# Optimization experiments

Measured on AMD Instinct MI355X. Metric: run time of the kernel, lower is better.

The kernel has to match this reference:

```python
import jax, jax.numpy as jnp
import numpy as np

BN_EPS = 1e-3  # Keras BatchNormalization default epsilon

def setup_inputs() -> dict:
    key = jax.random.key(0)
    ks = jax.random.split(key, 6)
    B, H, W, C = 8, 128, 128, 128
    s = 0.05  # small init scale for weights
    return {
        "x1": jax.random.normal(ks[0], (B, H, W, C), jnp.float32),
        "x2": jax.random.normal(ks[1], (B, H, W, C), jnp.float32),
        "Wq": jax.random.normal(ks[2], (C, C), jnp.float32) * s,
        "Wk": jax.random.normal(ks[3], (C, C), jnp.float32) * s,
        "Wv": jax.random.normal(ks[4], (C, C), jnp.float32) * s,
        "Ws": jax.random.normal(ks[5], (C, C), jnp.float32) * s,
        "bs": jnp.zeros((C,), jnp.float32),
        "scale": jnp.ones((1,), jnp.float32),   # layers.Attention use_scale=True, init 1
        "gamma": jnp.ones((C,), jnp.float32),
        "beta": jnp.zeros((C,), jnp.float32),
        "mu": jnp.zeros((C,), jnp.float32),
        "var": jnp.ones((C,), jnp.float32),
    }


def reference(x1, x2, Wq, Wk, Wv, Ws, bs, scale, gamma, beta, mu, var):
    # x1, x2: [B,H,W,C].  1x1 convs with relu == per-pixel channel matmul.
    q = jax.nn.relu(jnp.einsum('bhwc,cd->bhwd', x1, Wq))  # [B,H,W,C]
    k = jax.nn.relu(jnp.einsum('bhwc,cd->bhwd', x1, Wk))
    v = jax.nn.relu(jnp.einsum('bhwc,cd->bhwd', x2, Wv))
    # After transpose [0,3,1,2], Keras Attention batches over (B,C):
    # seq axis = H (rows), feature dim = W (cols). Fold the transposes into einsum.
    scores = scale[0] * jnp.einsum('bhwc,bgwc->bchg', q, k)  # [B,C,H,H]
    attn = jax.nn.softmax(scores, axis=-1)
    # attn @ v over row axis g, then implicit transpose back to NHWC.
    o = jnp.einsum('bchg,bgwc->bhwc', attn, v)  # [B,H,W,C]
    # sigmoid 1x1 conv (with bias), then inference-mode BatchNorm.
    g = jax.nn.sigmoid(jnp.einsum('bhwc,cd->bhwd', o, Ws) + bs)
    g = gamma * (g - mu) * jax.lax.rsqrt(var + BN_EPS) + beta
    # gated residual
    return x1 + x2 * g
```

## Files before the change

### kernel.cpp

```cpp
#include <hip/hip_runtime.h>

typedef unsigned int u32;
typedef unsigned short u16;
typedef u16 u16x4 __attribute__((ext_vector_type(4)));
typedef u16 u16x8 __attribute__((ext_vector_type(8)));
typedef u32 u32x2 __attribute__((ext_vector_type(2)));
typedef u32 u32x4 __attribute__((ext_vector_type(4)));
typedef __bf16 bf16x8 __attribute__((ext_vector_type(8)));
typedef float f32x4 __attribute__((ext_vector_type(4)));

#define LDK 136
#define TIDX(r, c) ((r) * LDK + ((c) ^ (((r) & 3) << 5)))
#define MFMA(a, b, c) __builtin_amdgcn_mfma_f32_16x16x32_bf16(a, b, c, 0, 0, 0)

__device__ __forceinline__ u16 f2b(float f) {
  u32 u = __builtin_bit_cast(u32, f);
  u = (u + 0x7fffu + ((u >> 16) & 1u)) >> 16;
  return (u16)u;
}
__device__ __forceinline__ float b2f(u16 h) {
  u32 u = ((u32)h) << 16;
  return __builtin_bit_cast(float, u);
}
__device__ __forceinline__ u32 pk2(float lo, float hi) {
  return (u32)f2b(lo) | ((u32)f2b(hi) << 16);
}

__global__ void wprep(const float* __restrict__ Wq, const float* __restrict__ Wk,
                      const float* __restrict__ Wv, const float* __restrict__ Ws,
                      u16* __restrict__ wT) {
  const float* srcs[4] = {Wq, Wk, Wv, Ws};
  const float* s = srcs[blockIdx.x];
  u16* d = wT + (size_t)blockIdx.x * 16384;
  for (int idx = threadIdx.x; idx < 16384; idx += 256) {
    int i = idx >> 7, j = idx & 127;
    d[j * 128 + i] = f2b(s[idx]);
  }
}

__global__ __launch_bounds__(256, 4)
void qkv_kernel(const float* __restrict__ x1, const float* __restrict__ x2,
                const u16* __restrict__ wT,
                u16* __restrict__ q_t, u16* __restrict__ k_t, u16* __restrict__ v_t) {
  __shared__ u16 Xs[128 * LDK];

  const int t = threadIdx.x;
  const int bid = blockIdx.x;
  const int xs = bid & 7;
  const int m = (bid >> 3) % 3;
  const int bh = (bid / 24) * 8 + xs;
  const int b = bh >> 7, h = bh & 127;
  const size_t pixbase = (size_t)bh * 16384;
  const size_t obase = (size_t)b * 2097152 + (size_t)h * 128;

  const float* xin = (m == 2) ? x2 : x1;
  u16* dst = (m == 0) ? q_t : (m == 1) ? k_t : v_t;

  const int lane = t & 63, wave = t >> 6;
  const int lrow = lane & 15, lq = lane >> 4;
  const int nstrip = wave * 32;

#pragma unroll
  for (int j = 0; j < 8; ++j) {
    int lin = j * 256 + t;
    int w = lin >> 4, c0 = (lin & 15) << 3;
    f32x4 a0 = *(const f32x4*)&xin[pixbase + lin * 8];
    f32x4 a1 = *(const f32x4*)&xin[pixbase + lin * 8 + 4];
    u16x8 p;
#pragma unroll
    for (int i = 0; i < 4; ++i) { p[i] = f2b(a0[i]); p[4 + i] = f2b(a1[i]); }
    *(u16x8*)&Xs[TIDX(w, c0)] = p;
  }

  const u16* wb = wT + (size_t)m * 16384;
  bf16x8 w0[4], w1[4];
#pragma unroll
  for (int kk = 0; kk < 4; ++kk) {
    int ko = kk * 32 + lq * 8;
    w0[kk] = *(const bf16x8*)&wb[(nstrip + lrow) * 128 + ko];
    w1[kk] = *(const bf16x8*)&wb[(nstrip + 16 + lrow) * 128 + ko];
  }
  __syncthreads();

  f32x4 acc[8][2];
#pragma unroll
  for (int mt = 0; mt < 8; ++mt) {
    acc[mt][0] = (f32x4){0.f, 0.f, 0.f, 0.f};
    acc[mt][1] = (f32x4){0.f, 0.f, 0.f, 0.f};
  }
#pragma unroll
  for (int kk = 0; kk < 4; ++kk) {
    int ko = kk * 32 + lq * 8;
#pragma unroll
    for (int mt = 0; mt < 8; ++mt) {
      bf16x8 a = *(const bf16x8*)&Xs[TIDX(mt * 16 + lrow, ko)];
      acc[mt][0] = MFMA(a, w0[kk], acc[mt][0]);
      acc[mt][1] = MFMA(a, w1[kk], acc[mt][1]);
    }
  }
  __syncthreads();

#pragma unroll
  for (int mt = 0; mt < 8; ++mt) {
    int w0i = mt * 16 + lq * 4;
#pragma unroll
    for (int nt = 0; nt < 2; ++nt) {
      int c = nstrip + nt * 16 + lrow;
      u32x2 p;
      p[0] = pk2(fmaxf(acc[mt][nt][0], 0.f), fmaxf(acc[mt][nt][1], 0.f));
      p[1] = pk2(fmaxf(acc[mt][nt][2], 0.f), fmaxf(acc[mt][nt][3], 0.f));
      *(u32x2*)&Xs[TIDX(c, w0i)] = p;
    }
  }
  __syncthreads();

#pragma unroll
  for (int j = 0; j < 8; ++j) {
    int c = j * 16 + (t >> 4), wv = (t & 15) * 8;
    *(u16x8*)&dst[obase + (size_t)c * 16384 + wv] = *(const u16x8*)&Xs[TIDX(c, wv)];
  }
}

__global__ __launch_bounds__(256, 3)
void attn_kernel(u16* __restrict__ q_t, const u16* __restrict__ k_t,
                 const u16* __restrict__ v_t, const float* __restrict__ scale_p) {
  __shared__ u16 Ks[128 * LDK];

  const int t = threadIdx.x;
  const size_t base = (size_t)blockIdx.x * 16384;

  const int lane = t & 63, wave = t >> 6;
  const int lrow = lane & 15, lq = lane >> 4;
  const int hstrip = wave * 32;
  const float scl = scale_p[0];

  bf16x8 q0[4], q1[4];
#pragma unroll
  for (int kk = 0; kk < 4; ++kk) {
    int ko = kk * 32 + lq * 8;
    q0[kk] = *(const bf16x8*)&q_t[base + (hstrip + lrow) * 128 + ko];
    q1[kk] = *(const bf16x8*)&q_t[base + (hstrip + 16 + lrow) * 128 + ko];
  }
#pragma unroll
  for (int j = 0; j < 8; ++j) {
    int lin = j * 256 + t;
    int r = lin >> 4, c0 = (lin & 15) << 3;
    *(u16x8*)&Ks[TIDX(r, c0)] = *(const u16x8*)&k_t[base + lin * 8];
  }
  __syncthreads();

  f32x4 acc[8][2];
#pragma unroll
  for (int mt = 0; mt < 8; ++mt) {
    acc[mt][0] = (f32x4){0.f, 0.f, 0.f, 0.f};
    acc[mt][1] = (f32x4){0.f, 0.f, 0.f, 0.f};
  }
#pragma unroll
  for (int kk = 0; kk < 4; ++kk) {
    int ko = kk * 32 + lq * 8;
#pragma unroll
    for (int mt = 0; mt < 8; ++mt) {
      bf16x8 a = *(const bf16x8*)&Ks[TIDX(mt * 16 + lrow, ko)];
      acc[mt][0] = MFMA(a, q0[kk], acc[mt][0]);
      acc[mt][1] = MFMA(a, q1[kk], acc[mt][1]);
    }
  }

  const int w0v = (t & 15) * 8, g0 = (t >> 4) * 8;
  u16x8 vv[8];
#pragma unroll
  for (int i = 0; i < 8; ++i)
    vv[i] = *(const u16x8*)&v_t[base + (size_t)(g0 + i) * 128 + w0v];

  float inv[2];
#pragma unroll
  for (int nt = 0; nt < 2; ++nt) {
    float mx = -1e30f;
#pragma unroll
    for (int mt = 0; mt < 8; ++mt)
#pragma unroll
      for (int r = 0; r < 4; ++r) {
        acc[mt][nt][r] *= scl;
        mx = fmaxf(mx, acc[mt][nt][r]);
      }
    mx = fmaxf(mx, __shfl_xor(mx, 16));
    mx = fmaxf(mx, __shfl_xor(mx, 32));
    float s = 0.f;
#pragma unroll
    for (int mt = 0; mt < 8; ++mt)
#pragma unroll
      for (int r = 0; r < 4; ++r) {
        float e = __expf(acc[mt][nt][r] - mx);
        acc[mt][nt][r] = e;
        s += e;
      }
    s += __shfl_xor(s, 16);
    s += __shfl_xor(s, 32);
    inv[nt] = 1.f / s;
  }

  u32 pk[8][2][2];
#pragma unroll
  for (int mt = 0; mt < 8; ++mt)
#pragma unroll
    for (int nt = 0; nt < 2; ++nt) {
      pk[mt][nt][0] = pk2(acc[mt][nt][0] * inv[nt], acc[mt][nt][1] * inv[nt]);
      pk[mt][nt][1] = pk2(acc[mt][nt][2] * inv[nt], acc[mt][nt][3] * inv[nt]);
    }
  __syncthreads();

#pragma unroll
  for (int j = 0; j < 8; ++j) {
    u16x8 tv;
#pragma unroll
    for (int i = 0; i < 8; ++i) tv[i] = vv[i][j];
    *(u16x8*)&Ks[TIDX(w0v + j, g0)] = tv;
  }
  __syncthreads();

  const int s01 = lrow + 32 * (lq & 1);
  const int s23 = s01 + 16;
  const bool hi = (lq & 2);
#pragma unroll
  for (int kk = 0; kk < 4; ++kk) {
    int ko = kk * 32 + lq * 8;
    u32x4 bd[2];
#pragma unroll
    for (int nt = 0; nt < 2; ++nt) {
      u32 a0 = pk[2 * kk][nt][0], a1 = pk[2 * kk][nt][1];
      u32 c0 = pk[2 * kk + 1][nt][0], c1 = pk[2 * kk + 1][nt][1];
      u32 l0 = (u32)__shfl((int)a0, s01), h0 = (u32)__shfl((int)c0, s01);
      u32 l1 = (u32)__shfl((int)a1, s01), h1 = (u32)__shfl((int)c1, s01);
      u32 l2 = (u32)__shfl((int)a0, s23), h2 = (u32)__shfl((int)c0, s23);
      u32 l3 = (u32)__shfl((int)a1, s23), h3 = (u32)__shfl((int)c1, s23);
      bd[nt][0] = hi ? h0 : l0;
      bd[nt][1] = hi ? h1 : l1;
      bd[nt][2] = hi ? h2 : l2;
      bd[nt][3] = hi ? h3 : l3;
    }
    bf16x8 bb0 = __builtin_bit_cast(bf16x8, bd[0]);
    bf16x8 bb1 = __builtin_bit_cast(bf16x8, bd[1]);
    if (kk == 0) {
#pragma unroll
      for (int mt = 0; mt < 8; ++mt) {
        acc[mt][0] = (f32x4){0.f, 0.f, 0.f, 0.f};
        acc[mt][1] = (f32x4){0.f, 0.f, 0.f, 0.f};
      }
    }
#pragma unroll
    for (int mt = 0; mt < 8; ++mt) {
      bf16x8 a = *(const bf16x8*)&Ks[TIDX(mt * 16 + lrow, ko)];
      acc[mt][0] = MFMA(a, bb0, acc[mt][0]);
      acc[mt][1] = MFMA(a, bb1, acc[mt][1]);
    }
  }
  __syncthreads();

#pragma unroll
  for (int mt = 0; mt < 8; ++mt) {
    int w0i = mt * 16 + lq * 4;
#pragma unroll
    for (int nt = 0; nt < 2; ++nt) {
      int hh = hstrip + nt * 16 + lrow;
      u32x2 p;
      p[0] = pk2(acc[mt][nt][0], acc[mt][nt][1]);
      p[1] = pk2(acc[mt][nt][2], acc[mt][nt][3]);
      *(u32x2*)&Ks[TIDX(hh, w0i)] = p;
    }
  }
  __syncthreads();
#pragma unroll
  for (int j = 0; j < 8; ++j) {
    int hh = j * 16 + (t >> 4), wv = (t & 15) * 8;
    *(u16x8*)&q_t[base + hh * 128 + wv] = *(const u16x8*)&Ks[TIDX(hh, wv)];
  }
}

__global__ __launch_bounds__(256, 4)
void final_kernel(const u16* __restrict__ o_t, const u16* __restrict__ wsT,
                  const float* __restrict__ x1, const float* __restrict__ x2,
                  const float* __restrict__ bs, const float* __restrict__ gamma,
                  const float* __restrict__ beta, const float* __restrict__ mu,
                  const float* __restrict__ var, float* __restrict__ out) {
  __shared__ u16 Os[128 * LDK];
  __shared__ float bnA[128], bnB[128], bsf[128];

  const int t = threadIdx.x;
  const int bh = blockIdx.x;
  const int b = bh >> 7, h = bh & 127;
  const size_t obase = (size_t)b * 2097152 + (size_t)h * 128;
  const size_t pixbase = (size_t)bh * 16384;

  if (t < 128) {
    float a = gamma[t] * rsqrtf(var[t] + 1e-3f);
    bnA[t] = a;
    bnB[t] = beta[t] - mu[t] * a;
    bsf[t] = bs[t];
  }
  {
    int cb = (t >> 4) * 8, w0 = (t & 15) * 8;
    u16 ov[8][8];
#pragma unroll
    for (int i = 0; i < 8; ++i)
      *(u16x8*)&ov[i][0] = *(const u16x8*)&o_t[obase + (size_t)(cb + i) * 16384 + w0];
#pragma unroll
    for (int j = 0; j < 8; ++j) {
      u16x8 tv;
#pragma unroll
      for (int i = 0; i < 8; ++i) tv[i] = ov[i][j];
      *(u16x8*)&Os[TIDX(w0 + j, cb)] = tv;
    }
  }
  __syncthreads();

  const int lane = t & 63, wave = t >> 6;
  const int lrow = lane & 15, lq = lane >> 4;
  const int wstrip = wave * 32;

  f32x4 acc[8][2];
#pragma unroll
  for (int mt = 0; mt < 8; ++mt) {
    acc[mt][0] = (f32x4){0.f, 0.f, 0.f, 0.f};
    acc[mt][1] = (f32x4){0.f, 0.f, 0.f, 0.f};
  }
#pragma unroll
  for (int kk = 0; kk < 4; ++kk) {
    int ko = kk * 32 + lq * 8;
    bf16x8 b0 = *(const bf16x8*)&Os[TIDX(wstrip + lrow, ko)];
    bf16x8 b1 = *(const bf16x8*)&Os[TIDX(wstrip + 16 + lrow, ko)];
#pragma unroll
    for (int mt = 0; mt < 8; ++mt) {
      bf16x8 a = *(const bf16x8*)&wsT[(mt * 16 + lrow) * 128 + ko];
      acc[mt][0] = MFMA(a, b0, acc[mt][0]);
      acc[mt][1] = MFMA(a, b1, acc[mt][1]);
    }
  }

#pragma unroll
  for (int mt = 0; mt < 8; ++mt) {
    int d0 = mt * 16 + lq * 4;
    f32x4 A4 = *(const f32x4*)&bnA[d0];
    f32x4 B4 = *(const f32x4*)&bnB[d0];
    f32x4 S4 = *(const f32x4*)&bsf[d0];
#pragma unroll
    for (int nt = 0; nt < 2; ++nt) {
      int w = wstrip + nt * 16 + lrow;
      size_t off = pixbase + (size_t)w * 128 + d0;
      f32x4 a1v = *(const f32x4*)&x1[off];
      f32x4 a2v = *(const f32x4*)&x2[off];
      f32x4 r;
#pragma unroll
      for (int r4 = 0; r4 < 4; ++r4) {
        float sv = acc[mt][nt][r4] + S4[r4];
        float sg = 1.f / (1.f + __expf(-sv));
        float g = A4[r4] * sg + B4[r4];
        r[r4] = a1v[r4] + a2v[r4] * g;
      }
      *(f32x4*)&out[off] = r;
    }
  }
}

extern "C" void kernel_launch(void* const* d_in, const int* in_sizes, int n_in,
                              void* d_out, int out_size, void* d_ws, size_t ws_size,
                              hipStream_t stream) {
  const float* x1 = (const float*)d_in[0];
  const float* x2 = (const float*)d_in[1];
  const float* Wq = (const float*)d_in[2];
  const float* Wk = (const float*)d_in[3];
  const float* Wv = (const float*)d_in[4];
  const float* Ws = (const float*)d_in[5];
  const float* bs = (const float*)d_in[6];
  const float* scale = (const float*)d_in[7];
  const float* gamma = (const float*)d_in[8];
  const float* beta = (const float*)d_in[9];
  const float* mu = (const float*)d_in[10];
  const float* var = (const float*)d_in[11];
  float* outp = (float*)d_out;

  u16* q_t = (u16*)d_ws;
  u16* k_t = q_t + 16777216;
  u16* v_t = k_t + 16777216;
  u16* wT = v_t + 16777216;

  wprep<<<dim3(4), dim3(256), 0, stream>>>(Wq, Wk, Wv, Ws, wT);
  qkv_kernel<<<dim3(3072), dim3(256), 0, stream>>>(x1, x2, wT, q_t, k_t, v_t);
  attn_kernel<<<dim3(1024), dim3(256), 0, stream>>>(q_t, k_t, v_t, scale);
  final_kernel<<<dim3(1024), dim3(256), 0, stream>>>(q_t, wT + 3 * 16384, x1, x2, bs,
                                                     gamma, beta, mu, var, outp);
}
```

Before: 322.8 us.

## Split qkv and final kernel blocks into half-row tiles for higher occupancy

Both the QKV projection and the final gating kernel now process 64 pixels of a row per block instead of 128. This halves LDS use and accumulator registers, doubles the grid, and raises launch bounds to 8 blocks per CU. The aim is more latency hiding on the memory-bound fp32 loads and stores. In exchange, the final kernel's weight loads are split across waves by output-channel strip, the qkv epilogue uses an unswizzled LDS layout with narrower writes, and global stores for o_t/q_t rows become 64-element halves.

```diff
diff --git a/kernel.cpp b/kernel.cpp
--- a/kernel.cpp
+++ b/kernel.cpp
@@ -38,20 +38,21 @@
   }
 }
 
-__global__ __launch_bounds__(256, 4)
+__global__ __launch_bounds__(256, 8)
 void qkv_kernel(const float* __restrict__ x1, const float* __restrict__ x2,
                 const u16* __restrict__ wT,
                 u16* __restrict__ q_t, u16* __restrict__ k_t, u16* __restrict__ v_t) {
-  __shared__ u16 Xs[128 * LDK];
+  __shared__ u16 Xs[64 * LDK];
 
   const int t = threadIdx.x;
   const int bid = blockIdx.x;
   const int xs = bid & 7;
-  const int m = (bid >> 3) % 3;
-  const int bh = (bid / 24) * 8 + xs;
+  const int mh = (bid >> 3) % 6;
+  const int m = mh % 3, half = mh / 3;
+  const int bh = (bid / 48) * 8 + xs;
   const int b = bh >> 7, h = bh & 127;
-  const size_t pixbase = (size_t)bh * 16384;
-  const size_t obase = (size_t)b * 2097152 + (size_t)h * 128;
+  const size_t pixbase = (size_t)bh * 16384 + half * 8192;
+  const size_t obase = (size_t)b * 2097152 + (size_t)h * 128 + half * 64;
 
   const float* xin = (m == 2) ? x2 : x1;
   u16* dst = (m == 0) ? q_t : (m == 1) ? k_t : v_t;
@@ -61,7 +62,7 @@
   const int nstrip = wave * 32;
 
 #pragma unroll
-  for (int j = 0; j < 8; ++j) {
+  for (int j = 0; j < 4; ++j) {
     int lin = j * 256 + t;
     int w = lin >> 4, c0 = (lin & 15) << 3;
     f32x4 a0 = *(const f32x4*)&xin[pixbase + lin * 8];
@@ -82,9 +83,9 @@
   }
   __syncthreads();
 
-  f32x4 acc[8][2];
-#pragma unroll
-  for (int mt = 0; mt < 8; ++mt) {
+  f32x4 acc[4][2];
+#pragma unroll
+  for (int mt = 0; mt < 4; ++mt) {
     acc[mt][0] = (f32x4){0.f, 0.f, 0.f, 0.f};
     acc[mt][1] = (f32x4){0.f, 0.f, 0.f, 0.f};
   }
@@ -92,7 +93,7 @@
   for (int kk = 0; kk < 4; ++kk) {
     int ko = kk * 32 + lq * 8;
 #pragma unroll
-    for (int mt = 0; mt < 8; ++mt) {
+    for (int mt = 0; mt < 4; ++mt) {
       bf16x8 a = *(const bf16x8*)&Xs[TIDX(mt * 16 + lrow, ko)];
       acc[mt][0] = MFMA(a, w0[kk], acc[mt][0]);
       acc[mt][1] = MFMA(a, w1[kk], acc[mt][1]);
@@ -101,7 +102,7 @@
   __syncthreads();
 
 #pragma unroll
-  for (int mt = 0; mt < 8; ++mt) {
+  for (int mt = 0; mt < 4; ++mt) {
     int w0i = mt * 16 + lq * 4;
 #pragma unroll
     for (int nt = 0; nt < 2; ++nt) {
@@ -109,15 +110,18 @@
       u32x2 p;
       p[0] = pk2(fmaxf(acc[mt][nt][0], 0.f), fmaxf(acc[mt][nt][1], 0.f));
       p[1] = pk2(fmaxf(acc[mt][nt][2], 0.f), fmaxf(acc[mt][nt][3], 0.f));
-      *(u32x2*)&Xs[TIDX(c, w0i)] = p;
-    }
-  }
-  __syncthreads();
-
-#pragma unroll
-  for (int j = 0; j < 8; ++j) {
-    int c = j * 16 + (t >> 4), wv = (t & 15) * 8;
-    *(u16x8*)&dst[obase + (size_t)c * 16384 + wv] = *(const u16x8*)&Xs[TIDX(c, wv)];
+      *(u32x2*)&Xs[c * 68 + w0i] = p;
+    }
+  }
+  __syncthreads();
+
+#pragma unroll
+  for (int j = 0; j < 4; ++j) {
+    int c = j * 32 + (t >> 3), wv = (t & 7) * 8;
+    u32x2 lo = *(const u32x2*)&Xs[c * 68 + wv];
+    u32x2 hi = *(const u32x2*)&Xs[c * 68 + wv + 4];
+    u32x4 full = {lo[0], lo[1], hi[0], hi[1]};
+    *(u32x4*)&dst[obase + (size_t)c * 16384 + wv] = full;
   }
 }
 
@@ -276,20 +280,21 @@
   }
 }
 
-__global__ __launch_bounds__(256, 4)
+__global__ __launch_bounds__(256, 8)
 void final_kernel(const u16* __restrict__ o_t, const u16* __restrict__ wsT,
                   const float* __restrict__ x1, const float* __restrict__ x2,
                   const float* __restrict__ bs, const float* __restrict__ gamma,
                   const float* __restrict__ beta, const float* __restrict__ mu,
                   const float* __restrict__ var, float* __restrict__ out) {
-  __shared__ u16 Os[128 * LDK];
+  __shared__ u16 Os[64 * LDK];
   __shared__ float bnA[128], bnB[128], bsf[128];
 
   const int t = threadIdx.x;
-  const int bh = blockIdx.x;
+  const int bid = blockIdx.x;
+  const int bh = bid >> 1, half = bid & 1;
   const int b = bh >> 7, h = bh & 127;
-  const size_t obase = (size_t)b * 2097152 + (size_t)h * 128;
-  const size_t pixbase = (size_t)bh * 16384;
+  const size_t obase = (size_t)b * 2097152 + (size_t)h * 128 + half * 64;
+  const size_t pixbase = (size_t)bh * 16384 + half * 8192;
 
   if (t < 128) {
     float a = gamma[t] * rsqrtf(var[t] + 1e-3f);
@@ -298,28 +303,29 @@
     bsf[t] = bs[t];
   }
   {
-    int cb = (t >> 4) * 8, w0 = (t & 15) * 8;
-    u16 ov[8][8];
+    int c0 = (t >> 4) * 8, w0 = (t & 15) * 4;
+    u16x4 ov[8];
 #pragma unroll
     for (int i = 0; i < 8; ++i)
-      *(u16x8*)&ov[i][0] = *(const u16x8*)&o_t[obase + (size_t)(cb + i) * 16384 + w0];
-#pragma unroll
-    for (int j = 0; j < 8; ++j) {
+      ov[i] = *(const u16x4*)&o_t[obase + (size_t)(c0 + i) * 16384 + w0];
+#pragma unroll
+    for (int j = 0; j < 4; ++j) {
       u16x8 tv;
 #pragma unroll
       for (int i = 0; i < 8; ++i) tv[i] = ov[i][j];
-      *(u16x8*)&Os[TIDX(w0 + j, cb)] = tv;
+      *(u16x8*)&Os[TIDX(w0 + j, c0)] = tv;
     }
   }
   __syncthreads();
 
   const int lane = t & 63, wave = t >> 6;
   const int lrow = lane & 15, lq = lane >> 4;
-  const int wstrip = wave * 32;
-
-  f32x4 acc[8][2];
-#pragma unroll
-  for (int mt = 0; mt < 8; ++mt) {
+  const int dstrip = (wave >> 1) * 64;
+  const int wstrip = (wave & 1) * 32;
+
+  f32x4 acc[4][2];
+#pragma unroll
+  for (int mt = 0; mt < 4; ++mt) {
     acc[mt][0] = (f32x4){0.f, 0.f, 0.f, 0.f};
     acc[mt][1] = (f32x4){0.f, 0.f, 0.f, 0.f};
   }
@@ -329,16 +335,16 @@
     bf16x8 b0 = *(const bf16x8*)&Os[TIDX(wstrip + lrow, ko)];
     bf16x8 b1 = *(const bf16x8*)&Os[TIDX(wstrip + 16 + lrow, ko)];
 #pragma unroll
-    for (int mt = 0; mt < 8; ++mt) {
-      bf16x8 a = *(const bf16x8*)&wsT[(mt * 16 + lrow) * 128 + ko];
+    for (int mt = 0; mt < 4; ++mt) {
+      bf16x8 a = *(const bf16x8*)&wsT[(dstrip + mt * 16 + lrow) * 128 + ko];
       acc[mt][0] = MFMA(a, b0, acc[mt][0]);
       acc[mt][1] = MFMA(a, b1, acc[mt][1]);
     }
   }
 
 #pragma unroll
-  for (int mt = 0; mt < 8; ++mt) {
-    int d0 = mt * 16 + lq * 4;
+  for (int mt = 0; mt < 4; ++mt) {
+    int d0 = dstrip + mt * 16 + lq * 4;
     f32x4 A4 = *(const f32x4*)&bnA[d0];
     f32x4 B4 = *(const f32x4*)&bnB[d0];
     f32x4 S4 = *(const f32x4*)&bsf[d0];
@@ -384,8 +390,8 @@
   u16* wT = v_t + 16777216;
 
   wprep<<<dim3(4), dim3(256), 0, stream>>>(Wq, Wk, Wv, Ws, wT);
-  qkv_kernel<<<dim3(3072), dim3(256), 0, stream>>>(x1, x2, wT, q_t, k_t, v_t);
+  qkv_kernel<<<dim3(6144), dim3(256), 0, stream>>>(x1, x2, wT, q_t, k_t, v_t);
   attn_kernel<<<dim3(1024), dim3(256), 0, stream>>>(q_t, k_t, v_t, scale);
-  final_kernel<<<dim3(1024), dim3(256), 0, stream>>>(q_t, wT + 3 * 16384, x1, x2, bs,
+  final_kernel<<<dim3(2048), dim3(256), 0, stream>>>(q_t, wT + 3 * 16384, x1, x2, bs,
                                                      gamma, beta, mu, var, outp);
 }
```

After: 344.3 us. 6.7% more time.

## Load projection input fragments directly from global memory, skipping LDS staging

Applied to the files above, without the earlier changes.

The QKV projection kernel no longer stages the input tile in shared memory. Each wave now reads its own 32 pixel rows straight from global memory into MFMA A-fragments and converts them to bf16 in registers. It streams weight B-fragments from global for all 128 output channels, and the work split changes from channel strips to pixel strips. This drops one LDS round-trip and two barriers. In exchange, the global loads are strided per lane and less coalesced, and weights are re-read from global (likely L1/L2 hits) with no latency hiding.

```diff
diff --git a/kernel.cpp b/kernel.cpp
--- a/kernel.cpp
+++ b/kernel.cpp
@@ -58,57 +58,49 @@
 
   const int lane = t & 63, wave = t >> 6;
   const int lrow = lane & 15, lq = lane >> 4;
-  const int nstrip = wave * 32;
-
-#pragma unroll
-  for (int j = 0; j < 8; ++j) {
-    int lin = j * 256 + t;
-    int w = lin >> 4, c0 = (lin & 15) << 3;
-    f32x4 a0 = *(const f32x4*)&xin[pixbase + lin * 8];
-    f32x4 a1 = *(const f32x4*)&xin[pixbase + lin * 8 + 4];
-    u16x8 p;
-#pragma unroll
-    for (int i = 0; i < 4; ++i) { p[i] = f2b(a0[i]); p[4 + i] = f2b(a1[i]); }
-    *(u16x8*)&Xs[TIDX(w, c0)] = p;
-  }
-
   const u16* wb = wT + (size_t)m * 16384;
-  bf16x8 w0[4], w1[4];
-#pragma unroll
-  for (int kk = 0; kk < 4; ++kk) {
-    int ko = kk * 32 + lq * 8;
-    w0[kk] = *(const bf16x8*)&wb[(nstrip + lrow) * 128 + ko];
-    w1[kk] = *(const bf16x8*)&wb[(nstrip + 16 + lrow) * 128 + ko];
-  }
-  __syncthreads();
-
-  f32x4 acc[8][2];
-#pragma unroll
-  for (int mt = 0; mt < 8; ++mt) {
-    acc[mt][0] = (f32x4){0.f, 0.f, 0.f, 0.f};
-    acc[mt][1] = (f32x4){0.f, 0.f, 0.f, 0.f};
-  }
-#pragma unroll
-  for (int kk = 0; kk < 4; ++kk) {
-    int ko = kk * 32 + lq * 8;
-#pragma unroll
-    for (int mt = 0; mt < 8; ++mt) {
-      bf16x8 a = *(const bf16x8*)&Xs[TIDX(mt * 16 + lrow, ko)];
-      acc[mt][0] = MFMA(a, w0[kk], acc[mt][0]);
-      acc[mt][1] = MFMA(a, w1[kk], acc[mt][1]);
-    }
-  }
-  __syncthreads();
-
-#pragma unroll
-  for (int mt = 0; mt < 8; ++mt) {
-    int w0i = mt * 16 + lq * 4;
-#pragma unroll
-    for (int nt = 0; nt < 2; ++nt) {
-      int c = nstrip + nt * 16 + lrow;
+
+  const float* arow0 = &xin[pixbase + (size_t)(wave * 32 + lrow) * 128];
+  const float* arow1 = arow0 + 16 * 128;
+
+  f32x4 acc[2][8];
+#pragma unroll
+  for (int mt = 0; mt < 2; ++mt)
+#pragma unroll
+    for (int ns = 0; ns < 8; ++ns) acc[mt][ns] = (f32x4){0.f, 0.f, 0.f, 0.f};
+
+#pragma unroll
+  for (int kk = 0; kk < 4; ++kk) {
+    int ko = kk * 32 + lq * 8;
+    f32x4 u00 = *(const f32x4*)&arow0[ko];
+    f32x4 u01 = *(const f32x4*)&arow0[ko + 4];
+    f32x4 u10 = *(const f32x4*)&arow1[ko];
+    f32x4 u11 = *(const f32x4*)&arow1[ko + 4];
+    u16x8 pa0, pa1;
+#pragma unroll
+    for (int i = 0; i < 4; ++i) {
+      pa0[i] = f2b(u00[i]); pa0[4 + i] = f2b(u01[i]);
+      pa1[i] = f2b(u10[i]); pa1[4 + i] = f2b(u11[i]);
+    }
+    bf16x8 a0 = __builtin_bit_cast(bf16x8, pa0);
+    bf16x8 a1 = __builtin_bit_cast(bf16x8, pa1);
+#pragma unroll
+    for (int ns = 0; ns < 8; ++ns) {
+      bf16x8 bfrag = *(const bf16x8*)&wb[(ns * 16 + lrow) * 128 + ko];
+      acc[0][ns] = MFMA(a0, bfrag, acc[0][ns]);
+      acc[1][ns] = MFMA(a1, bfrag, acc[1][ns]);
+    }
+  }
+
+#pragma unroll
+  for (int mt = 0; mt < 2; ++mt) {
+    int w0i = wave * 32 + mt * 16 + lq * 4;
+#pragma unroll
+    for (int ns = 0; ns < 8; ++ns) {
+      int c = ns * 16 + lrow;
       u32x2 p;
-      p[0] = pk2(fmaxf(acc[mt][nt][0], 0.f), fmaxf(acc[mt][nt][1], 0.f));
-      p[1] = pk2(fmaxf(acc[mt][nt][2], 0.f), fmaxf(acc[mt][nt][3], 0.f));
+      p[0] = pk2(fmaxf(acc[mt][ns][0], 0.f), fmaxf(acc[mt][ns][1], 0.f));
+      p[1] = pk2(fmaxf(acc[mt][ns][2], 0.f), fmaxf(acc[mt][ns][3], 0.f));
       *(u32x2*)&Xs[TIDX(c, w0i)] = p;
     }
   }
```

After: 348.6 us. +8.0%, slower.
